# Optimization experiments

Hardware: AMD Instinct MI355X
Metric: run time of the kernel (lower is better)

The kernel has to match this reference:

```python
import jax, jax.numpy as jnp
import numpy as np

NUM_HEADS = 8
MAX_POINTS = 8


def _sample_one(img, x, y):
    # img: [hd, Hs, Ws]; x, y: [N, P] pixel coords. Bilinear, zeros padding,
    # align_corners=True (caller already converted normalized coords to pixels).
    Hs, Ws = img.shape[-2], img.shape[-1]
    x0f = jnp.floor(x); y0f = jnp.floor(y)
    x0 = x0f.astype(jnp.int32); y0 = y0f.astype(jnp.int32)
    x1 = x0 + 1; y1 = y0 + 1
    wx1 = x - x0f; wx0 = 1.0 - wx1
    wy1 = y - y0f; wy0 = 1.0 - wy1

    def gather(yi, xi):
        valid = ((yi >= 0) & (yi < Hs) & (xi >= 0) & (xi < Ws)).astype(img.dtype)
        yc = jnp.clip(yi, 0, Hs - 1)
        xc = jnp.clip(xi, 0, Ws - 1)
        return img[:, yc, xc] * valid  # [hd, N, P]

    return (gather(y0, x0) * (wy0 * wx0) + gather(y0, x1) * (wy0 * wx1)
            + gather(y1, x0) * (wy1 * wx0) + gather(y1, x1) * (wy1 * wx1))


def _forward(query, ref, q_w, q_b, kv_w, kv_b, off_w, off_b, out_w, out_b, H, W, n_points):
    B, N, C = query.shape
    hd = C // NUM_HEADS
    scale = hd ** -0.5

    q = (query @ q_w + q_b).reshape(B, N, NUM_HEADS, hd)
    # kv_proj is dead code in the source forward (k, v are never used); params kept for parity.

    offsets = (query @ off_w + off_b).reshape(B, N, NUM_HEADS, MAX_POINTS, 2)
    offsets = offsets[:, :, :, :n_points]  # [B, N, nh, P, 2]

    ys = jnp.arange(H, dtype=query.dtype)
    xs = jnp.arange(W, dtype=query.dtype)
    coords = jnp.stack(jnp.meshgrid(ys, xs, indexing='ij'), -1).reshape(N, 2)  # (y, x)
    loc = coords[None, :, None, None, :] + offsets  # [B, N, nh, P, 2]
    g0 = loc[..., 0] / (H - 1) * 2.0 - 1.0
    g1 = loc[..., 1] / (W - 1) * 2.0 - 1.0
    # grid_sample reads grid[...,0] as x and grid[...,1] as y -> faithful to the
    # source's coordinate-channel ordering (channel 0 was normalized with H).
    x_pix = (g0 + 1.0) * 0.5 * (W - 1)
    y_pix = (g1 + 1.0) * 0.5 * (H - 1)

    ref_img = ref.reshape(B, C, H, W)  # faithful to source's .view (raw reinterpret, no permute)
    ref_heads = ref_img.reshape(B, NUM_HEADS, hd, H, W)  # per-head channel slice

    xb = x_pix.transpose(0, 2, 1, 3)  # [B, nh, N, P]
    yb = y_pix.transpose(0, 2, 1, 3)
    sampled = jax.vmap(jax.vmap(_sample_one))(ref_heads, xb, yb)  # [B, nh, hd, N, P]
    sampled = sampled.transpose(0, 3, 1, 4, 2)  # [B, N, nh, P, hd]

    attn = jax.nn.softmax(jnp.einsum('bnhd,bnhpd->bnhp', q, sampled) * scale, axis=-1)
    out = jnp.einsum('bnhp,bnhpd->bnhd', attn, sampled).reshape(B, N, C)
    return out @ out_w + out_b


def setup_inputs():
    key = jax.random.key(0)
    B, H, W, C = 4, 64, 64, 512
    N = H * W
    ks = jax.random.split(key, 8)
    w = lambda k, shp: jax.random.normal(k, shp, jnp.float32) * 0.02
    return {
        'query': jax.random.normal(ks[0], (B, N, C), jnp.float32),
        'ref': jax.random.normal(ks[1], (B, N, C), jnp.float32),
        'q_w': w(ks[2], (C, C)), 'q_b': jnp.zeros((C,), jnp.float32),
        'kv_w': w(ks[3], (C, 2 * C)), 'kv_b': jnp.zeros((2 * C,), jnp.float32),
        'off_w': w(ks[4], (C, NUM_HEADS * MAX_POINTS * 2)),
        'off_b': jnp.zeros((NUM_HEADS * MAX_POINTS * 2,), jnp.float32),
        'out_w': w(ks[5], (C, C)), 'out_b': jnp.zeros((C,), jnp.float32),
        'H': H, 'W': W, 'n_points': 8,
    }


def reference(query, ref, q_w, q_b, kv_w, kv_b, off_w, off_b, out_w, out_b, H, W, n_points):
    return _forward(query, ref, q_w, q_b, kv_w, kv_b, off_w, off_b, out_w, out_b, H, W, n_points)
```

## Files before the change

kernel.cpp:

```cpp
#include <hip/hip_runtime.h>
#include <cmath>

#define NUM_HEADS 8
#define MAX_POINTS 8
#define HD 64

typedef short bf16x8 __attribute__((ext_vector_type(8)));
typedef float f32x4 __attribute__((ext_vector_type(4)));

__device__ __forceinline__ unsigned short f2bf(float f) {
    unsigned u = __float_as_uint(f);
    unsigned r = (u + 0x7fff + ((u >> 16) & 1)) >> 16;
    return (unsigned short)r;
}
__device__ __forceinline__ float bf2f(unsigned short s) {
    return __uint_as_float(((unsigned)s) << 16);
}

__global__ __launch_bounds__(256) void cvt_bf16_k(
    const float* __restrict__ in, unsigned short* __restrict__ out, int n)
{
    int i = (blockIdx.x * 256 + threadIdx.x) * 4;
    if (i >= n) return;
    float4 v = *(const float4*)&in[i];
    ushort4 o;
    o.x = f2bf(v.x); o.y = f2bf(v.y); o.z = f2bf(v.z); o.w = f2bf(v.w);
    *(ushort4*)&out[i] = o;
}

__global__ __launch_bounds__(256) void tconv_w_k(
    const float* __restrict__ in, unsigned short* __restrict__ out, int K, int N)
{
    __shared__ float tile[32][33];
    int k0 = blockIdx.x * 32, n0 = blockIdx.y * 32;
    int tx = threadIdx.x, ty = threadIdx.y;
#pragma unroll
    for (int i = 0; i < 32; i += 8)
        tile[ty + i][tx] = in[(size_t)(k0 + ty + i) * N + n0 + tx];
    __syncthreads();
#pragma unroll
    for (int i = 0; i < 32; i += 8)
        out[(size_t)(n0 + ty + i) * K + k0 + tx] = f2bf(tile[tx][ty + i]);
}

__global__ __launch_bounds__(256) void transpose_ref_k(
    const float* __restrict__ in, float* __restrict__ out, int C, int S)
{
    __shared__ float tile[32][33];
    int b = blockIdx.z;
    int c0 = blockIdx.x * 32;
    int s0 = blockIdx.y * 32;
    int tx = threadIdx.x, ty = threadIdx.y;
    const float* ib = in + (size_t)b * C * S;
    float* ob = out + (size_t)b * S * C;
#pragma unroll
    for (int i = 0; i < 32; i += 8)
        tile[ty + i][tx] = ib[(size_t)(c0 + ty + i) * S + s0 + tx];
    __syncthreads();
#pragma unroll
    for (int i = 0; i < 32; i += 8)
        ob[(size_t)(s0 + ty + i) * C + c0 + tx] = tile[tx][ty + i];
}

#define LDK 40

__global__ __launch_bounds__(256) void gemm_bf16_mfma(
    const unsigned short* __restrict__ A, const unsigned short* __restrict__ BT,
    const float* __restrict__ bias, float* __restrict__ Cf,
    unsigned short* __restrict__ Cb, int M, int N, int K)
{
    __shared__ unsigned short As[64 * LDK];
    __shared__ unsigned short Bs[64 * LDK];
    int tid = threadIdx.x;
    int wave = tid >> 6, lane = tid & 63;
    int quad = lane >> 4, l16 = lane & 15;
    int bm = blockIdx.y * 64, bn = blockIdx.x * 64;
    int wm = (wave >> 1) * 32, wn = (wave & 1) * 32;

    int srow = tid >> 2, schunk = (tid & 3) * 8;

    f32x4 acc[2][2];
#pragma unroll
    for (int i = 0; i < 2; ++i)
#pragma unroll
        for (int j = 0; j < 2; ++j)
            acc[i][j] = (f32x4){0.f, 0.f, 0.f, 0.f};

    for (int k0 = 0; k0 < K; k0 += 32) {
        *(uint4*)&As[srow * LDK + schunk] =
            *(const uint4*)&A[(size_t)(bm + srow) * K + k0 + schunk];
        *(uint4*)&Bs[srow * LDK + schunk] =
            *(const uint4*)&BT[(size_t)(bn + srow) * K + k0 + schunk];
        __syncthreads();
        bf16x8 af[2], bfr[2];
#pragma unroll
        for (int t = 0; t < 2; ++t) {
            af[t]  = *(const bf16x8*)&As[(wm + t * 16 + l16) * LDK + quad * 8];
            bfr[t] = *(const bf16x8*)&Bs[(wn + t * 16 + l16) * LDK + quad * 8];
        }
#pragma unroll
        for (int mt = 0; mt < 2; ++mt)
#pragma unroll
            for (int nt = 0; nt < 2; ++nt)
                acc[mt][nt] = __builtin_amdgcn_mfma_f32_16x16x32_bf16(
                    af[mt], bfr[nt], acc[mt][nt], 0, 0, 0);
        __syncthreads();
    }

#pragma unroll
    for (int mt = 0; mt < 2; ++mt)
#pragma unroll
        for (int nt = 0; nt < 2; ++nt) {
            int r0 = bm + wm + mt * 16 + quad * 4;
            int c  = bn + wn + nt * 16 + l16;
            float bv = bias[c];
#pragma unroll
            for (int r = 0; r < 4; ++r) {
                float v = acc[mt][nt][r] + bv;
                if (Cf) Cf[(size_t)(r0 + r) * N + c] = v;
                if (Cb) Cb[(size_t)(r0 + r) * N + c] = f2bf(v);
            }
        }
}

__global__ __launch_bounds__(256) void sample_attn4_k(
    const unsigned short* __restrict__ qb, const float* __restrict__ offb,
    const float* __restrict__ refT, unsigned short* __restrict__ ob,
    const int* __restrict__ Hp, const int* __restrict__ Wp,
    const int* __restrict__ npp, int B, int N, int C)
{
    int H = *Hp, W = *Wp, npts = *npp;
    int wid = blockIdx.x * 4 + (threadIdx.x >> 6);
    int lane = threadIdx.x & 63;
    int hg = wid & 1;
    int bn = wid >> 1;
    int b = bn / N, n = bn % N;
    int h = hg * 4 + (lane >> 4);
    int c4 = (lane & 15) * 4;
    int coff = h * HD + c4;
    int row = n / W, col = n % W;

    ushort4 qs = *(const ushort4*)&qb[(size_t)bn * C + coff];
    float q0 = bf2f(qs.x), q1 = bf2f(qs.y), q2 = bf2f(qs.z), q3 = bf2f(qs.w);

    const float* op = offb + (size_t)bn * (NUM_HEADS * MAX_POINTS * 2)
                    + h * (MAX_POINTS * 2);
    const float* rb = refT + (size_t)b * ((size_t)H * W) * C;

    float rX = (H > 1) ? (float)(W - 1) / (float)(H - 1) : 0.f;
    float rY = (W > 1) ? (float)(H - 1) / (float)(W - 1) : 0.f;

    f32x4 sv[MAX_POINTS];
    float lg[MAX_POINTS];
#pragma unroll
    for (int p = 0; p < MAX_POINTS; ++p) {
        float off0 = op[p * 2 + 0];
        float off1 = op[p * 2 + 1];
        float x = ((float)row + off0) * rX;
        float y = ((float)col + off1) * rY;
        float x0f = floorf(x), y0f = floorf(y);
        int x0 = (int)x0f, y0 = (int)y0f;
        float wx1 = x - x0f, wx0 = 1.f - wx1;
        float wy1 = y - y0f, wy0 = 1.f - wy1;

        f32x4 v = (f32x4){0.f, 0.f, 0.f, 0.f};
#pragma unroll
        for (int t = 0; t < 4; ++t) {
            int yi = y0 + (t >> 1);
            int xi = x0 + (t & 1);
            float wgt = ((t >> 1) ? wy1 : wy0) * ((t & 1) ? wx1 : wx0);
            bool ok = (yi >= 0) & (yi < H) & (xi >= 0) & (xi < W);
            float wv = ok ? wgt : 0.f;
            int yc = min(max(yi, 0), H - 1);
            int xc = min(max(xi, 0), W - 1);
            const f32x4 src = *(const f32x4*)&rb[((size_t)yc * W + xc) * C + coff];
            v += wv * src;
        }
        sv[p] = v;
        float t = q0 * v[0] + q1 * v[1] + q2 * v[2] + q3 * v[3];
        t += __shfl_xor(t, 1);
        t += __shfl_xor(t, 2);
        t += __shfl_xor(t, 4);
        t += __shfl_xor(t, 8);
        lg[p] = (p < npts) ? t * 0.125f : -1e30f;
    }

    float mx = -1e30f;
#pragma unroll
    for (int p = 0; p < MAX_POINTS; ++p) mx = fmaxf(mx, lg[p]);
    float ssum = 0.f;
#pragma unroll
    for (int p = 0; p < MAX_POINTS; ++p) {
        lg[p] = __expf(lg[p] - mx);
        ssum += lg[p];
    }
    float inv = 1.f / ssum;
    f32x4 outv = (f32x4){0.f, 0.f, 0.f, 0.f};
#pragma unroll
    for (int p = 0; p < MAX_POINTS; ++p) outv += lg[p] * sv[p];

    ushort4 o;
    o.x = f2bf(outv[0] * inv); o.y = f2bf(outv[1] * inv);
    o.z = f2bf(outv[2] * inv); o.w = f2bf(outv[3] * inv);
    *(ushort4*)&ob[(size_t)bn * C + coff] = o;
}

extern "C" void kernel_launch(void* const* d_in, const int* in_sizes, int n_in,
                              void* d_out, int out_size, void* d_ws, size_t ws_size,
                              hipStream_t stream) {
    const float* query = (const float*)d_in[0];
    const float* ref   = (const float*)d_in[1];
    const float* q_w   = (const float*)d_in[2];
    const float* q_b   = (const float*)d_in[3];
    const float* off_w = (const float*)d_in[6];
    const float* off_b = (const float*)d_in[7];
    const float* out_w = (const float*)d_in[8];
    const float* out_b = (const float*)d_in[9];
    const int* Hp   = (const int*)d_in[10];
    const int* Wp   = (const int*)d_in[11];
    const int* npp  = (const int*)d_in[12];

    const int C = 512;
    const int B = 4;
    const int H = 64, W = 64;
    const int N = H * W;
    const int M = B * N;
    const int OFFD = NUM_HEADS * MAX_POINTS * 2;

    float* refT   = (float*)d_ws;
    float* offbuf = refT + (size_t)M * C;
    unsigned short* qin_bf  = (unsigned short*)(offbuf + (size_t)M * OFFD);
    unsigned short* qbuf_bf = qin_bf  + (size_t)M * C;
    unsigned short* obuf_bf = qbuf_bf + (size_t)M * C;
    unsigned short* wqT     = obuf_bf + (size_t)M * C;
    unsigned short* woffT   = wqT   + (size_t)C * C;
    unsigned short* woutT   = woffT + (size_t)OFFD * C;

    dim3 blk(256);
    cvt_bf16_k<<<dim3((M * C) / 1024), blk, 0, stream>>>(query, qin_bf, M * C);
    tconv_w_k<<<dim3(C / 32, C / 32), dim3(32, 8), 0, stream>>>(q_w, wqT, C, C);
    tconv_w_k<<<dim3(C / 32, OFFD / 32), dim3(32, 8), 0, stream>>>(off_w, woffT, C, OFFD);
    tconv_w_k<<<dim3(C / 32, C / 32), dim3(32, 8), 0, stream>>>(out_w, woutT, C, C);
    transpose_ref_k<<<dim3(C / 32, N / 32, B), dim3(32, 8), 0, stream>>>(ref, refT, C, N);

    gemm_bf16_mfma<<<dim3(C / 64, M / 64), blk, 0, stream>>>(
        qin_bf, wqT, q_b, nullptr, qbuf_bf, M, C, C);
    gemm_bf16_mfma<<<dim3(OFFD / 64, M / 64), blk, 0, stream>>>(
        qin_bf, woffT, off_b, offbuf, nullptr, M, OFFD, C);

    sample_attn4_k<<<dim3((M * 2) / 4), blk, 0, stream>>>(
        qbuf_bf, offbuf, refT, obuf_bf, Hp, Wp, npp, B, N, C);

    gemm_bf16_mfma<<<dim3(C / 64, M / 64), blk, 0, stream>>>(
        obuf_bf, woutT, out_b, (float*)d_out, nullptr, M, C, C);
}
```

Baseline: 248.8 us.

## Store ref in bf16, use 128x128 MFMA GEMM with direct LDS loads, widen sampler

The ref transpose now writes bf16 through a generalized batched transpose-convert kernel, which halves the bytes the bilinear sampler gathers. The sampler maps one wave per query over all 8 heads with 8 channels per lane, using 16-byte bf16 loads and one fewer shuffle step. The q and output projections switch to a 128x128-tile MFMA GEMM that fills LDS with global_load_lds, giving more reuse per block. The trade-offs are bf16 rounding of ref values, more accumulator registers in the GEMM, and fewer GEMM blocks.

```diff
diff --git a/kernel.cpp b/kernel.cpp
--- a/kernel.cpp
+++ b/kernel.cpp
@@ -7,6 +7,9 @@
 
 typedef short bf16x8 __attribute__((ext_vector_type(8)));
 typedef float f32x4 __attribute__((ext_vector_type(4)));
+
+typedef const __attribute__((address_space(1))) unsigned int gu32;
+typedef __attribute__((address_space(3))) unsigned int lu32;
 
 __device__ __forceinline__ unsigned short f2bf(float f) {
     unsigned u = __float_as_uint(f);
@@ -15,6 +18,15 @@
 }
 __device__ __forceinline__ float bf2f(unsigned short s) {
     return __uint_as_float(((unsigned)s) << 16);
+}
+__device__ __forceinline__ unsigned packbf2(float a, float b) {
+    return (unsigned)f2bf(a) | ((unsigned)f2bf(b) << 16);
+}
+__device__ __forceinline__ void unpack8(uint4 u, float* f) {
+    f[0] = __uint_as_float(u.x << 16); f[1] = __uint_as_float(u.x & 0xffff0000u);
+    f[2] = __uint_as_float(u.y << 16); f[3] = __uint_as_float(u.y & 0xffff0000u);
+    f[4] = __uint_as_float(u.z << 16); f[5] = __uint_as_float(u.z & 0xffff0000u);
+    f[6] = __uint_as_float(u.w << 16); f[7] = __uint_as_float(u.w & 0xffff0000u);
 }
 
 __global__ __launch_bounds__(256) void cvt_bf16_k(
@@ -28,43 +40,25 @@
     *(ushort4*)&out[i] = o;
 }
 
-__global__ __launch_bounds__(256) void tconv_w_k(
+__global__ __launch_bounds__(256) void tconv_k(
     const float* __restrict__ in, unsigned short* __restrict__ out, int K, int N)
 {
     __shared__ float tile[32][33];
+    size_t ib = (size_t)blockIdx.z * K * N;
     int k0 = blockIdx.x * 32, n0 = blockIdx.y * 32;
     int tx = threadIdx.x, ty = threadIdx.y;
 #pragma unroll
     for (int i = 0; i < 32; i += 8)
-        tile[ty + i][tx] = in[(size_t)(k0 + ty + i) * N + n0 + tx];
+        tile[ty + i][tx] = in[ib + (size_t)(k0 + ty + i) * N + n0 + tx];
     __syncthreads();
 #pragma unroll
     for (int i = 0; i < 32; i += 8)
-        out[(size_t)(n0 + ty + i) * K + k0 + tx] = f2bf(tile[tx][ty + i]);
-}
-
-__global__ __launch_bounds__(256) void transpose_ref_k(
-    const float* __restrict__ in, float* __restrict__ out, int C, int S)
-{
-    __shared__ float tile[32][33];
-    int b = blockIdx.z;
-    int c0 = blockIdx.x * 32;
-    int s0 = blockIdx.y * 32;
-    int tx = threadIdx.x, ty = threadIdx.y;
-    const float* ib = in + (size_t)b * C * S;
-    float* ob = out + (size_t)b * S * C;
-#pragma unroll
-    for (int i = 0; i < 32; i += 8)
-        tile[ty + i][tx] = ib[(size_t)(c0 + ty + i) * S + s0 + tx];
-    __syncthreads();
-#pragma unroll
-    for (int i = 0; i < 32; i += 8)
-        ob[(size_t)(s0 + ty + i) * C + c0 + tx] = tile[tx][ty + i];
+        out[ib + (size_t)(n0 + ty + i) * K + k0 + tx] = f2bf(tile[tx][ty + i]);
 }
 
 #define LDK 40
 
-__global__ __launch_bounds__(256) void gemm_bf16_mfma(
+__global__ __launch_bounds__(256) void gemm_bf16_mfma64(
     const unsigned short* __restrict__ A, const unsigned short* __restrict__ BT,
     const float* __restrict__ bias, float* __restrict__ Cf,
     unsigned short* __restrict__ Cb, int M, int N, int K)
@@ -76,7 +70,6 @@
     int quad = lane >> 4, l16 = lane & 15;
     int bm = blockIdx.y * 64, bn = blockIdx.x * 64;
     int wm = (wave >> 1) * 32, wn = (wave & 1) * 32;
-
     int srow = tid >> 2, schunk = (tid & 3) * 8;
 
     f32x4 acc[2][2];
@@ -106,7 +99,6 @@
                     af[mt], bfr[nt], acc[mt][nt], 0, 0, 0);
         __syncthreads();
     }
-
 #pragma unroll
     for (int mt = 0; mt < 2; ++mt)
 #pragma unroll
@@ -123,34 +115,98 @@
         }
 }
 
-__global__ __launch_bounds__(256) void sample_attn4_k(
+__global__ __launch_bounds__(256) void gemm_bf16_mfma128(
+    const unsigned short* __restrict__ A, const unsigned short* __restrict__ BT,
+    const float* __restrict__ bias, float* __restrict__ Cf,
+    unsigned short* __restrict__ Cb, int M, int N, int K)
+{
+    __shared__ unsigned short As[128 * 32];
+    __shared__ unsigned short Bs[128 * 32];
+    int tid = threadIdx.x;
+    int wave = tid >> 6, lane = tid & 63;
+    int quad = lane >> 4, l16 = lane & 15;
+    int bm = blockIdx.y * 128, bn = blockIdx.x * 128;
+    int wm = (wave >> 1) * 64, wn = (wave & 1) * 64;
+
+    int srow = tid >> 2, sq = (tid & 3) * 8;
+    const unsigned short* aP0 = &A[(size_t)(bm + srow) * K + sq];
+    const unsigned short* aP1 = aP0 + (size_t)64 * K;
+    const unsigned short* bP0 = &BT[(size_t)(bn + srow) * K + sq];
+    const unsigned short* bP1 = bP0 + (size_t)64 * K;
+    lu32* aL0 = (lu32*)&As[wave * 512];
+    lu32* aL1 = (lu32*)&As[2048 + wave * 512];
+    lu32* bL0 = (lu32*)&Bs[wave * 512];
+    lu32* bL1 = (lu32*)&Bs[2048 + wave * 512];
+
+    f32x4 acc[4][4];
+#pragma unroll
+    for (int i = 0; i < 4; ++i)
+#pragma unroll
+        for (int j = 0; j < 4; ++j)
+            acc[i][j] = (f32x4){0.f, 0.f, 0.f, 0.f};
+
+    for (int k0 = 0; k0 < K; k0 += 32) {
+        __builtin_amdgcn_global_load_lds((gu32*)(aP0 + k0), aL0, 16, 0, 0);
+        __builtin_amdgcn_global_load_lds((gu32*)(aP1 + k0), aL1, 16, 0, 0);
+        __builtin_amdgcn_global_load_lds((gu32*)(bP0 + k0), bL0, 16, 0, 0);
+        __builtin_amdgcn_global_load_lds((gu32*)(bP1 + k0), bL1, 16, 0, 0);
+        __syncthreads();
+        bf16x8 af[4], bfr[4];
+#pragma unroll
+        for (int t = 0; t < 4; ++t) {
+            af[t]  = *(const bf16x8*)&As[(wm + t * 16 + l16) * 32 + quad * 8];
+            bfr[t] = *(const bf16x8*)&Bs[(wn + t * 16 + l16) * 32 + quad * 8];
+        }
+#pragma unroll
+        for (int mt = 0; mt < 4; ++mt)
+#pragma unroll
+            for (int nt = 0; nt < 4; ++nt)
+                acc[mt][nt] = __builtin_amdgcn_mfma_f32_16x16x32_bf16(
+                    af[mt], bfr[nt], acc[mt][nt], 0, 0, 0);
+        __syncthreads();
+    }
+
+#pragma unroll
+    for (int mt = 0; mt < 4; ++mt)
+#pragma unroll
+        for (int nt = 0; nt < 4; ++nt) {
+            int r0 = bm + wm + mt * 16 + quad * 4;
+            int c  = bn + wn + nt * 16 + l16;
+            float bv = bias[c];
+#pragma unroll
+            for (int r = 0; r < 4; ++r) {
+                float v = acc[mt][nt][r] + bv;
+                if (Cf) Cf[(size_t)(r0 + r) * N + c] = v;
+                if (Cb) Cb[(size_t)(r0 + r) * N + c] = f2bf(v);
+            }
+        }
+}
+
+__global__ __launch_bounds__(256) void sample_attn8_k(
     const unsigned short* __restrict__ qb, const float* __restrict__ offb,
-    const float* __restrict__ refT, unsigned short* __restrict__ ob,
+    const unsigned short* __restrict__ refT, unsigned short* __restrict__ ob,
     const int* __restrict__ Hp, const int* __restrict__ Wp,
     const int* __restrict__ npp, int B, int N, int C)
 {
     int H = *Hp, W = *Wp, npts = *npp;
-    int wid = blockIdx.x * 4 + (threadIdx.x >> 6);
+    int bn = blockIdx.x * 4 + (threadIdx.x >> 6);
     int lane = threadIdx.x & 63;
-    int hg = wid & 1;
-    int bn = wid >> 1;
-    int b = bn / N, n = bn % N;
-    int h = hg * 4 + (lane >> 4);
-    int c4 = (lane & 15) * 4;
-    int coff = h * HD + c4;
-    int row = n / W, col = n % W;
-
-    ushort4 qs = *(const ushort4*)&qb[(size_t)bn * C + coff];
-    float q0 = bf2f(qs.x), q1 = bf2f(qs.y), q2 = bf2f(qs.z), q3 = bf2f(qs.w);
-
-    const float* op = offb + (size_t)bn * (NUM_HEADS * MAX_POINTS * 2)
-                    + h * (MAX_POINTS * 2);
-    const float* rb = refT + (size_t)b * ((size_t)H * W) * C;
+    int h = lane >> 3;
+    int c8 = (lane & 7) << 3;
+    int coff = (h << 6) + c8;
+    int b = bn / N, n = bn - b * N;
+    int row = n / W, col = n - row * W;
+
+    float qv[8];
+    unpack8(*(const uint4*)&qb[bn * C + coff], qv);
+
+    const float* op = offb + bn * (NUM_HEADS * MAX_POINTS * 2) + (h << 4);
+    const unsigned short* rb = refT + b * N * C;
 
     float rX = (H > 1) ? (float)(W - 1) / (float)(H - 1) : 0.f;
     float rY = (W > 1) ? (float)(H - 1) / (float)(W - 1) : 0.f;
 
-    f32x4 sv[MAX_POINTS];
+    float sv[MAX_POINTS][8];
     float lg[MAX_POINTS];
 #pragma unroll
     for (int p = 0; p < MAX_POINTS; ++p) {
@@ -163,25 +219,30 @@
         float wx1 = x - x0f, wx0 = 1.f - wx1;
         float wy1 = y - y0f, wy0 = 1.f - wy1;
 
-        f32x4 v = (f32x4){0.f, 0.f, 0.f, 0.f};
+        float a8[8] = {0.f, 0.f, 0.f, 0.f, 0.f, 0.f, 0.f, 0.f};
 #pragma unroll
         for (int t = 0; t < 4; ++t) {
             int yi = y0 + (t >> 1);
             int xi = x0 + (t & 1);
             float wgt = ((t >> 1) ? wy1 : wy0) * ((t & 1) ? wx1 : wx0);
-            bool ok = (yi >= 0) & (yi < H) & (xi >= 0) & (xi < W);
+            bool ok = ((unsigned)yi < (unsigned)H) & ((unsigned)xi < (unsigned)W);
             float wv = ok ? wgt : 0.f;
             int yc = min(max(yi, 0), H - 1);
             int xc = min(max(xi, 0), W - 1);
-            const f32x4 src = *(const f32x4*)&rb[((size_t)yc * W + xc) * C + coff];
-            v += wv * src;
-        }
-        sv[p] = v;
-        float t = q0 * v[0] + q1 * v[1] + q2 * v[2] + q3 * v[3];
+            float sf[8];
+            unpack8(*(const uint4*)&rb[(yc * W + xc) * C + coff], sf);
+#pragma unroll
+            for (int j = 0; j < 8; ++j) a8[j] = fmaf(wv, sf[j], a8[j]);
+        }
+        float t = 0.f;
+#pragma unroll
+        for (int j = 0; j < 8; ++j) {
+            sv[p][j] = a8[j];
+            t = fmaf(qv[j], a8[j], t);
+        }
         t += __shfl_xor(t, 1);
         t += __shfl_xor(t, 2);
         t += __shfl_xor(t, 4);
-        t += __shfl_xor(t, 8);
         lg[p] = (p < npts) ? t * 0.125f : -1e30f;
     }
 
@@ -195,14 +256,19 @@
         ssum += lg[p];
     }
     float inv = 1.f / ssum;
-    f32x4 outv = (f32x4){0.f, 0.f, 0.f, 0.f};
-#pragma unroll
-    for (int p = 0; p < MAX_POINTS; ++p) outv += lg[p] * sv[p];
-
-    ushort4 o;
-    o.x = f2bf(outv[0] * inv); o.y = f2bf(outv[1] * inv);
-    o.z = f2bf(outv[2] * inv); o.w = f2bf(outv[3] * inv);
-    *(ushort4*)&ob[(size_t)bn * C + coff] = o;
+
+    float o8[8] = {0.f, 0.f, 0.f, 0.f, 0.f, 0.f, 0.f, 0.f};
+#pragma unroll
+    for (int p = 0; p < MAX_POINTS; ++p)
+#pragma unroll
+        for (int j = 0; j < 8; ++j) o8[j] = fmaf(lg[p], sv[p][j], o8[j]);
+
+    uint4 o;
+    o.x = packbf2(o8[0] * inv, o8[1] * inv);
+    o.y = packbf2(o8[2] * inv, o8[3] * inv);
+    o.z = packbf2(o8[4] * inv, o8[5] * inv);
+    o.w = packbf2(o8[6] * inv, o8[7] * inv);
+    *(uint4*)&ob[bn * C + coff] = o;
 }
 
 extern "C" void kernel_launch(void* const* d_in, const int* in_sizes, int n_in,
@@ -227,9 +293,9 @@
     const int M = B * N;
     const int OFFD = NUM_HEADS * MAX_POINTS * 2;
 
-    float* refT   = (float*)d_ws;
-    float* offbuf = refT + (size_t)M * C;
-    unsigned short* qin_bf  = (unsigned short*)(offbuf + (size_t)M * OFFD);
+    float* offbuf = (float*)d_ws;
+    unsigned short* refT_bf = (unsigned short*)(offbuf + (size_t)M * OFFD);
+    unsigned short* qin_bf  = refT_bf + (size_t)M * C;
     unsigned short* qbuf_bf = qin_bf  + (size_t)M * C;
     unsigned short* obuf_bf = qbuf_bf + (size_t)M * C;
     unsigned short* wqT     = obuf_bf + (size_t)M * C;
@@ -238,19 +304,19 @@
 
     dim3 blk(256);
     cvt_bf16_k<<<dim3((M * C) / 1024), blk, 0, stream>>>(query, qin_bf, M * C);
-    tconv_w_k<<<dim3(C / 32, C / 32), dim3(32, 8), 0, stream>>>(q_w, wqT, C, C);
-    tconv_w_k<<<dim3(C / 32, OFFD / 32), dim3(32, 8), 0, stream>>>(off_w, woffT, C, OFFD);
-    tconv_w_k<<<dim3(C / 32, C / 32), dim3(32, 8), 0, stream>>>(out_w, woutT, C, C);
-    transpose_ref_k<<<dim3(C / 32, N / 32, B), dim3(32, 8), 0, stream>>>(ref, refT, C, N);
-
-    gemm_bf16_mfma<<<dim3(C / 64, M / 64), blk, 0, stream>>>(
+    tconv_k<<<dim3(C / 32, C / 32), dim3(32, 8), 0, stream>>>(q_w, wqT, C, C);
+    tconv_k<<<dim3(C / 32, OFFD / 32), dim3(32, 8), 0, stream>>>(off_w, woffT, C, OFFD);
+    tconv_k<<<dim3(C / 32, C / 32), dim3(32, 8), 0, stream>>>(out_w, woutT, C, C);
+    tconv_k<<<dim3(C / 32, N / 32, B), dim3(32, 8), 0, stream>>>(ref, refT_bf, C, N);
+
+    gemm_bf16_mfma128<<<dim3(C / 128, M / 128), blk, 0, stream>>>(
         qin_bf, wqT, q_b, nullptr, qbuf_bf, M, C, C);
-    gemm_bf16_mfma<<<dim3(OFFD / 64, M / 64), blk, 0, stream>>>(
+    gemm_bf16_mfma64<<<dim3(OFFD / 64, M / 64), blk, 0, stream>>>(
         qin_bf, woffT, off_b, offbuf, nullptr, M, OFFD, C);
 
-    sample_attn4_k<<<dim3((M * 2) / 4), blk, 0, stream>>>(
-        qbuf_bf, offbuf, refT, obuf_bf, Hp, Wp, npp, B, N, C);
-
-    gemm_bf16_mfma<<<dim3(C / 64, M / 64), blk, 0, stream>>>(
+    sample_attn8_k<<<dim3(M / 4), blk, 0, stream>>>(
+        qbuf_bf, offbuf, refT_bf, obuf_bf, Hp, Wp, npp, B, N, C);
+
+    gemm_bf16_mfma128<<<dim3(C / 128, M / 128), blk, 0, stream>>>(
         obuf_bf, woutT, out_b, (float*)d_out, nullptr, M, C, C);
 }
```

After: 224.7 us. 1.11x faster.
